# Kernel tuning notes

Measured on AMD Instinct MI355X. Metric: run time of the kernel, lower is better.

## Reference

```python
import jax, jax.numpy as jnp
import numpy as np

NUM_FEATURES = 5
MUL_FACTOR = 2.0


def setup_inputs() -> dict:
    key = jax.random.key(0)
    x = jax.random.normal(key, (4096, 512), dtype=jnp.float32)
    # buffer from __init__: mul_factor ** (arange(F) - F // 2)
    bandwidth_multipliers = (MUL_FACTOR ** (jnp.arange(NUM_FEATURES) - NUM_FEATURES // 2)).astype(jnp.float32)
    return {"x": x, "bandwidth_multipliers": bandwidth_multipliers}


def _cdist(x):
    # pairwise Euclidean distance, p=2
    sq = jnp.sum(x * x, axis=1)
    d2 = sq[:, None] + sq[None, :] - 2.0 * (x @ x.T)
    return jnp.sqrt(jnp.maximum(d2, 0.0))


def reference(x, bandwidth_multipliers):
    d = _cdist(x)  # [N, N]
    n = d.shape[0]
    # heuristic bandwidth on detached distances (self.bandwidth is None)
    bw = jax.lax.stop_gradient(d).sum() / (n * (n - 1))
    bws = bw * bandwidth_multipliers  # [F]
    # exp over F bandwidths, summed: [F, N, N] -> [N, N]
    return jnp.exp(-d[None, :, :] / bws[:, None, None]).sum(axis=0)
```

## Files before the change

kernel.cpp:

```cpp
#include <hip/hip_runtime.h>
#include <cstdint>
#include <cstddef>

#define N_PTS 4096
#define KDIM  512
#define NFEAT 5

typedef __attribute__((ext_vector_type(8))) short bf16x8;
typedef __attribute__((ext_vector_type(4))) float f32x4;

__device__ inline short f2bf(float f) {
  union { float f; uint32_t u; } v; v.f = f;
  uint32_t r = (v.u + 0x7fffu + ((v.u >> 16) & 1u)) >> 16;
  return (short)r;
}

__device__ inline void load_lds16(const void* g, void* l) {
  __builtin_amdgcn_global_load_lds(
      (const __attribute__((address_space(1))) void*)g,
      (__attribute__((address_space(3))) void*)l, 16, 0, 0);
}

__global__ __launch_bounds__(256) void prep_kernel(const float* __restrict__ X,
                                                   short* __restrict__ Xb,
                                                   float* __restrict__ sq) {
  const int row = blockIdx.x;
  const int t = threadIdx.x;
  const float2 v = ((const float2*)(X + (size_t)row * KDIM))[t];
  short2 b;
  b.x = f2bf(v.x);
  b.y = f2bf(v.y);
  ((short2*)(Xb + (size_t)row * KDIM))[t] = b;
  float s = v.x * v.x + v.y * v.y;
#pragma unroll
  for (int off = 32; off; off >>= 1) s += __shfl_down(s, off);
  __shared__ float ws[4];
  if ((t & 63) == 0) ws[t >> 6] = s;
  __syncthreads();
  if (t == 0) sq[row] = ws[0] + ws[1] + ws[2] + ws[3];
}

__global__ __launch_bounds__(256, 2) void dist_kernel(
    const short* __restrict__ Xb, const float* __restrict__ sq,
    float* __restrict__ D, float* __restrict__ gsum) {
  __shared__ short As[128 * 32];
  __shared__ short Bs[128 * 32];
  __shared__ float red[4];

  const int tid = threadIdx.x;
  const int lane = tid & 63;
  const int wid = tid >> 6;
  const int wave_m = wid >> 1, wave_n = wid & 1;
  const int lhi = lane >> 4, llo = lane & 15;
  const int bm = blockIdx.y, bn = blockIdx.x;

  f32x4 acc[4][4];
#pragma unroll
  for (int i = 0; i < 4; ++i)
#pragma unroll
    for (int j = 0; j < 4; ++j) acc[i][j] = (f32x4){0.f, 0.f, 0.f, 0.f};

  const int srow = tid >> 2;
  const int scol = (tid & 3) * 8;
  const size_t ga0 = (size_t)(bm * 128 + srow) * KDIM + scol;
  const size_t gb0 = (size_t)(bn * 128 + srow) * KDIM + scol;

  for (int kt = 0; kt < KDIM / 32; ++kt) {
    const int koff = kt * 32;
    load_lds16(Xb + ga0 + koff,             (char*)As + tid * 16);
    load_lds16(Xb + ga0 + 64 * KDIM + koff, (char*)As + 4096 + tid * 16);
    load_lds16(Xb + gb0 + koff,             (char*)Bs + tid * 16);
    load_lds16(Xb + gb0 + 64 * KDIM + koff, (char*)Bs + 4096 + tid * 16);
    __syncthreads();

    bf16x8 a[4], b[4];
#pragma unroll
    for (int i = 0; i < 4; ++i) {
      a[i] = *(const bf16x8*)&As[(wave_m * 64 + i * 16 + llo) * 32 + lhi * 8];
      b[i] = *(const bf16x8*)&Bs[(wave_n * 64 + i * 16 + llo) * 32 + lhi * 8];
    }
#pragma unroll
    for (int i = 0; i < 4; ++i)
#pragma unroll
      for (int j = 0; j < 4; ++j)
        acc[i][j] =
            __builtin_amdgcn_mfma_f32_16x16x32_bf16(a[i], b[j], acc[i][j], 0, 0, 0);
    __syncthreads();
  }

  float lsum = 0.f;
  const int gi0 = bm * 128 + wave_m * 64;
  const int gj0 = bn * 128 + wave_n * 64;
#pragma unroll
  for (int i = 0; i < 4; ++i) {
#pragma unroll
    for (int r = 0; r < 4; ++r) {
      const int gi = gi0 + i * 16 + lhi * 4 + r;
      const float sqi = sq[gi];
#pragma unroll
      for (int j = 0; j < 4; ++j) {
        const int gj = gj0 + j * 16 + llo;
        float d2 = sqi + sq[gj] - 2.f * acc[i][j][r];
        float dd = sqrtf(fmaxf(d2, 0.f));
        if (gi == gj) dd = 0.f;
        D[(size_t)gi * N_PTS + gj] = dd;
        lsum += dd;
      }
    }
  }
#pragma unroll
  for (int off = 32; off; off >>= 1) lsum += __shfl_down(lsum, off);
  if (lane == 0) red[wid] = lsum;
  __syncthreads();
  if (tid == 0) atomicAdd(gsum, red[0] + red[1] + red[2] + red[3]);
}

__global__ __launch_bounds__(256) void rbf_kernel(float* __restrict__ D,
                                                  const float* __restrict__ gsum,
                                                  const float* __restrict__ mult) {
  const float bw = *gsum * (1.0f / ((float)N_PTS * (float)(N_PTS - 1)));
  float c[NFEAT];
#pragma unroll
  for (int f = 0; f < NFEAT; ++f) c[f] = -1.0f / (bw * mult[f]);

  const size_t total = (size_t)N_PTS * N_PTS / 4;
  const size_t stride = (size_t)gridDim.x * blockDim.x;
  float4* D4 = (float4*)D;
  for (size_t idx = (size_t)blockIdx.x * blockDim.x + threadIdx.x; idx < total;
       idx += stride) {
    float4 v = D4[idx];
    float4 o = {0.f, 0.f, 0.f, 0.f};
#pragma unroll
    for (int f = 0; f < NFEAT; ++f) {
      o.x += __expf(v.x * c[f]);
      o.y += __expf(v.y * c[f]);
      o.z += __expf(v.z * c[f]);
      o.w += __expf(v.w * c[f]);
    }
    D4[idx] = o;
  }
}

extern "C" void kernel_launch(void* const* d_in, const int* in_sizes, int n_in,
                              void* d_out, int out_size, void* d_ws, size_t ws_size,
                              hipStream_t stream) {
  const float* X = (const float*)d_in[0];
  const float* mult = (const float*)d_in[1];
  float* D = (float*)d_out;

  char* ws = (char*)d_ws;
  float* gsum = (float*)ws;
  float* sq = (float*)(ws + 1024);
  short* Xb = (short*)(ws + 1024 + N_PTS * sizeof(float));

  hipMemsetAsync(gsum, 0, 256, stream);
  prep_kernel<<<N_PTS, 256, 0, stream>>>(X, Xb, sq);
  dist_kernel<<<dim3(N_PTS / 128, N_PTS / 128), 256, 0, stream>>>(Xb, sq, D, gsum);
  rbf_kernel<<<4096, 256, 0, stream>>>(D, gsum, mult);
}
```

Before: 130.5 us.

## Exploit distance symmetry, store bf16 intermediate distances, widen K tile

```diff
diff --git a/kernel.cpp b/kernel.cpp
--- a/kernel.cpp
+++ b/kernel.cpp
@@ -8,11 +8,18 @@
 
 typedef __attribute__((ext_vector_type(8))) short bf16x8;
 typedef __attribute__((ext_vector_type(4))) float f32x4;
-
-__device__ inline short f2bf(float f) {
-  union { float f; uint32_t u; } v; v.f = f;
-  uint32_t r = (v.u + 0x7fffu + ((v.u >> 16) & 1u)) >> 16;
-  return (short)r;
+typedef uint32_t u32;
+
+__device__ inline unsigned short f2bf(float f) {
+  union { float f; u32 u; } v; v.f = f;
+  u32 r = (v.u + 0x7fffu + ((v.u >> 16) & 1u)) >> 16;
+  return (unsigned short)r;
+}
+
+__device__ inline void bf2f2(u32 u, float& a, float& b) {
+  union { u32 u; float f; } x, y;
+  x.u = u << 16; y.u = u & 0xffff0000u;
+  a = x.f; b = y.f;
 }
 
 __device__ inline void load_lds16(const void* g, void* l) {
@@ -28,8 +35,8 @@
   const int t = threadIdx.x;
   const float2 v = ((const float2*)(X + (size_t)row * KDIM))[t];
   short2 b;
-  b.x = f2bf(v.x);
-  b.y = f2bf(v.y);
+  b.x = (short)f2bf(v.x);
+  b.y = (short)f2bf(v.y);
   ((short2*)(Xb + (size_t)row * KDIM))[t] = b;
   float s = v.x * v.x + v.y * v.y;
 #pragma unroll
@@ -42,9 +49,12 @@
 
 __global__ __launch_bounds__(256, 2) void dist_kernel(
     const short* __restrict__ Xb, const float* __restrict__ sq,
-    float* __restrict__ D, float* __restrict__ gsum) {
-  __shared__ short As[128 * 32];
-  __shared__ short Bs[128 * 32];
+    unsigned short* __restrict__ Dw, float* __restrict__ gsum) {
+  const int bm = blockIdx.y, bn = blockIdx.x;
+  if (bm > bn) return;
+
+  __shared__ short As[128 * 64];
+  __shared__ short Bs[128 * 64];
   __shared__ float red[4];
 
   const int tid = threadIdx.x;
@@ -52,7 +62,6 @@
   const int wid = tid >> 6;
   const int wave_m = wid >> 1, wave_n = wid & 1;
   const int lhi = lane >> 4, llo = lane & 15;
-  const int bm = blockIdx.y, bn = blockIdx.x;
 
   f32x4 acc[4][4];
 #pragma unroll
@@ -60,31 +69,36 @@
 #pragma unroll
     for (int j = 0; j < 4; ++j) acc[i][j] = (f32x4){0.f, 0.f, 0.f, 0.f};
 
-  const int srow = tid >> 2;
-  const int scol = (tid & 3) * 8;
+  const int srow = tid >> 3;
+  const int scol = (tid & 7) * 8;
   const size_t ga0 = (size_t)(bm * 128 + srow) * KDIM + scol;
   const size_t gb0 = (size_t)(bn * 128 + srow) * KDIM + scol;
 
-  for (int kt = 0; kt < KDIM / 32; ++kt) {
-    const int koff = kt * 32;
-    load_lds16(Xb + ga0 + koff,             (char*)As + tid * 16);
-    load_lds16(Xb + ga0 + 64 * KDIM + koff, (char*)As + 4096 + tid * 16);
-    load_lds16(Xb + gb0 + koff,             (char*)Bs + tid * 16);
-    load_lds16(Xb + gb0 + 64 * KDIM + koff, (char*)Bs + 4096 + tid * 16);
+  for (int kt = 0; kt < KDIM / 64; ++kt) {
+    const int koff = kt * 64;
+#pragma unroll
+    for (int g = 0; g < 4; ++g) {
+      load_lds16(Xb + ga0 + (size_t)g * 32 * KDIM + koff, (char*)As + g * 4096 + tid * 16);
+      load_lds16(Xb + gb0 + (size_t)g * 32 * KDIM + koff, (char*)Bs + g * 4096 + tid * 16);
+    }
     __syncthreads();
 
-    bf16x8 a[4], b[4];
-#pragma unroll
-    for (int i = 0; i < 4; ++i) {
-      a[i] = *(const bf16x8*)&As[(wave_m * 64 + i * 16 + llo) * 32 + lhi * 8];
-      b[i] = *(const bf16x8*)&Bs[(wave_n * 64 + i * 16 + llo) * 32 + lhi * 8];
-    }
-#pragma unroll
-    for (int i = 0; i < 4; ++i)
-#pragma unroll
-      for (int j = 0; j < 4; ++j)
-        acc[i][j] =
-            __builtin_amdgcn_mfma_f32_16x16x32_bf16(a[i], b[j], acc[i][j], 0, 0, 0);
+    bf16x8 a[2][4], b[2][4];
+#pragma unroll
+    for (int h = 0; h < 2; ++h)
+#pragma unroll
+      for (int i = 0; i < 4; ++i) {
+        a[h][i] = *(const bf16x8*)&As[(wave_m * 64 + i * 16 + llo) * 64 + h * 32 + lhi * 8];
+        b[h][i] = *(const bf16x8*)&Bs[(wave_n * 64 + i * 16 + llo) * 64 + h * 32 + lhi * 8];
+      }
+#pragma unroll
+    for (int h = 0; h < 2; ++h)
+#pragma unroll
+      for (int i = 0; i < 4; ++i)
+#pragma unroll
+        for (int j = 0; j < 4; ++j)
+          acc[i][j] =
+              __builtin_amdgcn_mfma_f32_16x16x32_bf16(a[h][i], b[h][j], acc[i][j], 0, 0, 0);
     __syncthreads();
   }
 
@@ -103,7 +117,7 @@
         float d2 = sqi + sq[gj] - 2.f * acc[i][j][r];
         float dd = sqrtf(fmaxf(d2, 0.f));
         if (gi == gj) dd = 0.f;
-        D[(size_t)gi * N_PTS + gj] = dd;
+        Dw[(size_t)gi * N_PTS + gj] = f2bf(dd);
         lsum += dd;
       }
     }
@@ -112,32 +126,77 @@
   for (int off = 32; off; off >>= 1) lsum += __shfl_down(lsum, off);
   if (lane == 0) red[wid] = lsum;
   __syncthreads();
-  if (tid == 0) atomicAdd(gsum, red[0] + red[1] + red[2] + red[3]);
-}
-
-__global__ __launch_bounds__(256) void rbf_kernel(float* __restrict__ D,
-                                                  const float* __restrict__ gsum,
-                                                  const float* __restrict__ mult) {
+  if (tid == 0) {
+    const float scale = (bm == bn) ? 1.f : 2.f;
+    atomicAdd(gsum, scale * (red[0] + red[1] + red[2] + red[3]));
+  }
+}
+
+__global__ __launch_bounds__(256) void rbf_kernel(
+    const unsigned short* __restrict__ Dw, const float* __restrict__ gsum,
+    const float* __restrict__ mult, float* __restrict__ out) {
+  const int bm = blockIdx.y, bn = blockIdx.x;
+  if (bm > bn) return;
+
+  __shared__ float S[32][132];
+
   const float bw = *gsum * (1.0f / ((float)N_PTS * (float)(N_PTS - 1)));
   float c[NFEAT];
 #pragma unroll
   for (int f = 0; f < NFEAT; ++f) c[f] = -1.0f / (bw * mult[f]);
 
-  const size_t total = (size_t)N_PTS * N_PTS / 4;
-  const size_t stride = (size_t)gridDim.x * blockDim.x;
-  float4* D4 = (float4*)D;
-  for (size_t idx = (size_t)blockIdx.x * blockDim.x + threadIdx.x; idx < total;
-       idx += stride) {
-    float4 v = D4[idx];
-    float4 o = {0.f, 0.f, 0.f, 0.f};
-#pragma unroll
-    for (int f = 0; f < NFEAT; ++f) {
-      o.x += __expf(v.x * c[f]);
-      o.y += __expf(v.y * c[f]);
-      o.z += __expf(v.z * c[f]);
-      o.w += __expf(v.w * c[f]);
-    }
-    D4[idx] = o;
+  const int t = threadIdx.x;
+  const int r = t >> 3;
+  const int c16 = (t & 7) * 16;
+  const int gj0 = bn * 128;
+  const int gi_base = bm * 128;
+
+  for (int s = 0; s < 4; ++s) {
+    const int gi = gi_base + s * 32 + r;
+    const unsigned short* src = Dw + (size_t)gi * N_PTS + gj0 + c16;
+    const uint4 p0 = *(const uint4*)src;
+    const uint4 p1 = *(const uint4*)(src + 8);
+
+    float v[16];
+    bf2f2(p0.x, v[0], v[1]);   bf2f2(p0.y, v[2], v[3]);
+    bf2f2(p0.z, v[4], v[5]);   bf2f2(p0.w, v[6], v[7]);
+    bf2f2(p1.x, v[8], v[9]);   bf2f2(p1.y, v[10], v[11]);
+    bf2f2(p1.z, v[12], v[13]); bf2f2(p1.w, v[14], v[15]);
+
+    float o[16];
+#pragma unroll
+    for (int e = 0; e < 16; ++e) {
+      float a = 0.f;
+#pragma unroll
+      for (int f = 0; f < NFEAT; ++f) a += __expf(v[e] * c[f]);
+      o[e] = a;
+    }
+
+    float* drow = out + (size_t)gi * N_PTS + gj0 + c16;
+#pragma unroll
+    for (int q = 0; q < 4; ++q)
+      ((float4*)drow)[q] = (float4){o[q * 4], o[q * 4 + 1], o[q * 4 + 2], o[q * 4 + 3]};
+
+    if (bm != bn) {
+#pragma unroll
+      for (int q = 0; q < 4; ++q)
+        *(float4*)&S[r][c16 + q * 4] =
+            (float4){o[q * 4], o[q * 4 + 1], o[q * 4 + 2], o[q * 4 + 3]};
+      __syncthreads();
+      const int tb = gi_base + s * 32;
+      const int k = t & 7;
+#pragma unroll
+      for (int p = 0; p < 4; ++p) {
+        const int cc = p * 32 + (t >> 3);
+        float4 q4;
+        q4.x = S[k * 4 + 0][cc];
+        q4.y = S[k * 4 + 1][cc];
+        q4.z = S[k * 4 + 2][cc];
+        q4.w = S[k * 4 + 3][cc];
+        *(float4*)&out[(size_t)(gj0 + cc) * N_PTS + tb + k * 4] = q4;
+      }
+      __syncthreads();
+    }
   }
 }
 
@@ -146,15 +205,17 @@
                               hipStream_t stream) {
   const float* X = (const float*)d_in[0];
   const float* mult = (const float*)d_in[1];
-  float* D = (float*)d_out;
+  float* out = (float*)d_out;
 
   char* ws = (char*)d_ws;
   float* gsum = (float*)ws;
   float* sq = (float*)(ws + 1024);
   short* Xb = (short*)(ws + 1024 + N_PTS * sizeof(float));
+  unsigned short* Dw = (unsigned short*)(ws + 1024 + N_PTS * sizeof(float) +
+                                         (size_t)N_PTS * KDIM * sizeof(short));
 
   hipMemsetAsync(gsum, 0, 256, stream);
   prep_kernel<<<N_PTS, 256, 0, stream>>>(X, Xb, sq);
-  dist_kernel<<<dim3(N_PTS / 128, N_PTS / 128), 256, 0, stream>>>(Xb, sq, D, gsum);
-  rbf_kernel<<<4096, 256, 0, stream>>>(D, gsum, mult);
-}
+  dist_kernel<<<dim3(32, 32), 256, 0, stream>>>(Xb, sq, Dw, gsum);
+  rbf_kernel<<<dim3(32, 32), 256, 0, stream>>>(Dw, gsum, mult, out);
+}
```

After: 134.6 us. 3.2% more time.
